# Performance work log

Hardware: AMD Instinct MI355X
Metric: run time of the kernel (lower is better)

The kernel has to match this reference:

```python
import jax, jax.numpy as jnp
import numpy as np

B, S, D = 2, 2048, 1024
H = 16
HD = D // H


def setup_inputs() -> dict:
    key = jax.random.key(0)
    k1, k2, k3 = jax.random.split(key, 3)
    x = jax.random.normal(k1, (B, S, D), dtype=jnp.float32)
    # nn.Linear(d, 3d, bias=False): weight [3d, d]; y = x @ W.T
    w_qkv = jax.random.normal(k2, (3 * D, D), dtype=jnp.float32) * (D ** -0.5)
    w_out = jax.random.normal(k3, (D, D), dtype=jnp.float32) * (D ** -0.5)
    return {"x": x, "w_qkv": w_qkv, "w_out": w_out}


def reference(x, w_qkv, w_out):
    batch, seq_len, _ = x.shape
    qkv = jnp.einsum('bsd,ed->bse', x, w_qkv)  # [B,S,3D]
    q, k, v = jnp.split(qkv, 3, axis=-1)
    # [B,S,D] -> [B,H,S,HD]
    def heads(t):
        return t.reshape(batch, seq_len, H, HD).transpose(0, 2, 1, 3)
    q, k, v = heads(q), heads(k), heads(v)
    scale = HD ** -0.5
    attn = jnp.einsum('bhqd,bhkd->bhqk', q, k) * scale  # [B,H,S,S]
    causal = jnp.triu(jnp.ones((seq_len, seq_len), dtype=bool), k=1)
    attn = jnp.where(causal, -jnp.inf, attn)
    attn = jax.nn.softmax(attn, axis=-1)
    out = jnp.einsum('bhqk,bhkd->bhqd', attn, v)  # [B,H,S,HD]
    out = out.transpose(0, 2, 1, 3).reshape(batch, seq_len, D)
    return jnp.einsum('bsd,ed->bse', out, w_out)
```

## Files before the change

### kernel.cpp

```cpp
#include <hip/hip_runtime.h>

#define NUM_B 2
#define SEQ   2048
#define DIM   1024
#define NH    16
#define HD    64

typedef __attribute__((ext_vector_type(8))) short short8;
typedef __attribute__((ext_vector_type(4))) float floatx4;
typedef unsigned short us;

#define SOFTMAX_SHIFT 12.0f

__device__ __forceinline__ us f2bf(float f) {
    unsigned u = __float_as_uint(f);
    u += 0x7fffu + ((u >> 16) & 1u);
    return (us)(u >> 16);
}
__device__ __forceinline__ us f2bf_t(float f) {
    return (us)(__float_as_uint(f) >> 16);
}

#define GLD16(gptr, lptr) __builtin_amdgcn_global_load_lds( \
    (__attribute__((address_space(1))) unsigned int*)(gptr), \
    (__attribute__((address_space(3))) unsigned int*)(lptr), 16, 0, 0)

__global__ __launch_bounds__(256) void cast_all(
    const float* __restrict__ x, const float* __restrict__ wq,
    const float* __restrict__ wo, us* __restrict__ xb,
    us* __restrict__ wqb, us* __restrict__ wob)
{
    int i = blockIdx.x * 256 + threadIdx.x;
    const float* src; us* dst; int off;
    if (i < 524288)      { src = x;  dst = xb;  off = i; }
    else if (i < 917504) { src = wq; dst = wqb; off = i - 524288; }
    else                 { src = wo; dst = wob; off = i - 917504; }
    const float4* p = (const float4*)src + (size_t)off * 2;
    float4 f0 = p[0];
    float4 f1 = p[1];
    short8 v;
    v[0] = (short)f2bf(f0.x); v[1] = (short)f2bf(f0.y);
    v[2] = (short)f2bf(f0.z); v[3] = (short)f2bf(f0.w);
    v[4] = (short)f2bf(f1.x); v[5] = (short)f2bf(f1.y);
    v[6] = (short)f2bf(f1.z); v[7] = (short)f2bf(f1.w);
    *(short8*)(dst + (size_t)off * 8) = v;
}

__global__ __launch_bounds__(256, 2) void gemm_qkv(
    const us* __restrict__ A, const us* __restrict__ Bw,
    us* __restrict__ qb, us* __restrict__ kb, us* __restrict__ vt)
{
    __shared__ us As[128 * 64];
    __shared__ us Bs[128 * 64];
    const int t = threadIdx.x;
    const int lane = t & 63, w = t >> 6;
    const int l16 = lane & 15, quad = lane >> 4;
    const int wr = (w >> 1) * 64, wc = (w & 1) * 64;
    const int m0 = blockIdx.y * 128, n0 = blockIdx.x * 128;
    const bool isV = (blockIdx.x >= 16);
    const int srow = lane >> 3;
    const int soff = ((lane & 7) ^ srow) << 3;
    const int rsw  = l16 & 7;

    floatx4 acc[4][4];
    #pragma unroll
    for (int i = 0; i < 4; ++i)
        #pragma unroll
        for (int j = 0; j < 4; ++j) acc[i][j] = (floatx4){0.f, 0.f, 0.f, 0.f};

    for (int k0 = 0; k0 < DIM; k0 += 64) {
        #pragma unroll
        for (int c = 0; c < 4; ++c) {
            int chunk = w * 4 + c;
            int row = chunk * 8 + srow;
            GLD16(A  + (size_t)(m0 + row) * DIM + k0 + soff, &As[chunk * 512]);
            GLD16(Bw + (size_t)(n0 + row) * DIM + k0 + soff, &Bs[chunk * 512]);
        }
        __syncthreads();
        #pragma unroll
        for (int s = 0; s < 2; ++s) {
            short8 af[4], bf[4];
            #pragma unroll
            for (int i = 0; i < 4; ++i)
                af[i] = *(const short8*)&As[(wr + i * 16 + l16) * 64 + (((s * 4 + quad) ^ rsw) << 3)];
            #pragma unroll
            for (int j = 0; j < 4; ++j)
                bf[j] = *(const short8*)&Bs[(wc + j * 16 + l16) * 64 + (((s * 4 + quad) ^ rsw) << 3)];
            if (!isV) {
                #pragma unroll
                for (int i = 0; i < 4; ++i)
                    #pragma unroll
                    for (int j = 0; j < 4; ++j)
                        acc[i][j] = __builtin_amdgcn_mfma_f32_16x16x32_bf16(af[i], bf[j], acc[i][j], 0, 0, 0);
            } else {
                #pragma unroll
                for (int i = 0; i < 4; ++i)
                    #pragma unroll
                    for (int j = 0; j < 4; ++j)
                        acc[i][j] = __builtin_amdgcn_mfma_f32_16x16x32_bf16(bf[j], af[i], acc[i][j], 0, 0, 0);
            }
        }
        __syncthreads();
    }

    if (!isV) {
        const int which = n0 >> 10;
        const float sc = (which == 0) ? 0.125f : 1.0f;
        us* dst = (which == 0) ? qb : kb;
        #pragma unroll
        for (int i = 0; i < 4; ++i) {
            #pragma unroll
            for (int j = 0; j < 4; ++j) {
                int e = n0 + wc + j * 16 + l16;
                int h  = (e >> 6) & 15;
                int hd = e & 63;
                #pragma unroll
                for (int r = 0; r < 4; ++r) {
                    int m = m0 + wr + i * 16 + quad * 4 + r;
                    int b = m >> 11, s = m & 2047;
                    dst[((size_t)((b * NH + h) * SEQ + s) << 6) + hd] = f2bf(acc[i][j][r] * sc);
                }
            }
        }
    } else {
        #pragma unroll
        for (int i = 0; i < 4; ++i) {
            int m = m0 + wr + i * 16 + l16;
            int b = m >> 11, s = m & 2047;
            #pragma unroll
            for (int j = 0; j < 4; ++j) {
                int e0 = (n0 - 2048) + wc + j * 16 + quad * 4;
                #pragma unroll
                for (int r = 0; r < 4; ++r) {
                    int e = e0 + r;
                    int h = e >> 6, hd = e & 63;
                    vt[((size_t)((b * NH + h) * HD + hd) << 11) + s] = f2bf(acc[i][j][r]);
                }
            }
        }
    }
}

__global__ __launch_bounds__(256, 2) void gemm_out(
    const us* __restrict__ A, const us* __restrict__ Bw, float* __restrict__ outp)
{
    __shared__ us As[64 * 64];
    __shared__ us Bs[128 * 64];
    const int t = threadIdx.x;
    const int lane = t & 63, w = t >> 6;
    const int l16 = lane & 15, quad = lane >> 4;
    const int wr = (w >> 1) * 32, wc = (w & 1) * 64;
    const int m0 = blockIdx.y * 64, n0 = blockIdx.x * 128;
    const int srow = lane >> 3;
    const int soff = ((lane & 7) ^ srow) << 3;
    const int rsw  = l16 & 7;

    floatx4 acc[2][4];
    #pragma unroll
    for (int i = 0; i < 2; ++i)
        #pragma unroll
        for (int j = 0; j < 4; ++j) acc[i][j] = (floatx4){0.f, 0.f, 0.f, 0.f};

    for (int k0 = 0; k0 < DIM; k0 += 64) {
        #pragma unroll
        for (int c = 0; c < 2; ++c) {
            int chunk = w * 2 + c;
            int row = chunk * 8 + srow;
            GLD16(A + (size_t)(m0 + row) * DIM + k0 + soff, &As[chunk * 512]);
        }
        #pragma unroll
        for (int c = 0; c < 4; ++c) {
            int chunk = w * 4 + c;
            int row = chunk * 8 + srow;
            GLD16(Bw + (size_t)(n0 + row) * DIM + k0 + soff, &Bs[chunk * 512]);
        }
        __syncthreads();
        #pragma unroll
        for (int s = 0; s < 2; ++s) {
            short8 af[2], bf[4];
            #pragma unroll
            for (int i = 0; i < 2; ++i)
                af[i] = *(const short8*)&As[(wr + i * 16 + l16) * 64 + (((s * 4 + quad) ^ rsw) << 3)];
            #pragma unroll
            for (int j = 0; j < 4; ++j)
                bf[j] = *(const short8*)&Bs[(wc + j * 16 + l16) * 64 + (((s * 4 + quad) ^ rsw) << 3)];
            #pragma unroll
            for (int i = 0; i < 2; ++i)
                #pragma unroll
                for (int j = 0; j < 4; ++j)
                    acc[i][j] = __builtin_amdgcn_mfma_f32_16x16x32_bf16(af[i], bf[j], acc[i][j], 0, 0, 0);
        }
        __syncthreads();
    }

    #pragma unroll
    for (int i = 0; i < 2; ++i)
        #pragma unroll
        for (int j = 0; j < 4; ++j) {
            int n = n0 + wc + j * 16 + l16;
            #pragma unroll
            for (int r = 0; r < 4; ++r) {
                int m = m0 + wr + i * 16 + quad * 4 + r;
                outp[(size_t)m * DIM + n] = acc[i][j][r];
            }
        }
}

__global__ __launch_bounds__(256, 4) void attn(
    const us* __restrict__ qb, const us* __restrict__ kb,
    const us* __restrict__ vt, us* __restrict__ ob)
{
    __shared__ us Ks[2][64 * 64];
    __shared__ us Vs[2][64 * 64];
    __shared__ us Ps[4 * 16 * 72];
    const int t = threadIdx.x;
    const int lane = t & 63, w = t >> 6;
    const int l16 = lane & 15, quad = lane >> 4;
    const int idx = blockIdx.x;
    const int qt = 31 - (idx >> 5);
    const int bh = idx & 31;
    const int b = bh >> 4, h = bh & 15;
    const int q0 = qt << 6;
    const int r0 = q0 + w * 16;
    const int rowb = r0 + quad * 4;
    const size_t base = (size_t)bh * SEQ * HD;
    const us* qbh = qb + base;
    const us* kbh = kb + base;
    const us* vth = vt + base;
    us* Pp = Ps + w * 16 * 72;
    const int srow = lane >> 3;
    const int soff = ((lane & 7) ^ srow) << 3;
    const int rsw  = l16 & 7;

    short8 qa[2];
    #pragma unroll
    for (int s = 0; s < 2; ++s)
        qa[s] = *(const short8*)(qbh + (size_t)(r0 + l16) * HD + s * 32 + quad * 8);

    floatx4 o[4];
    #pragma unroll
    for (int j = 0; j < 4; ++j) o[j] = (floatx4){0.f, 0.f, 0.f, 0.f};
    float lrow[4] = {0.f, 0.f, 0.f, 0.f};

    #pragma unroll
    for (int c = 0; c < 2; ++c) {
        int chunk = w * 2 + c;
        int row = chunk * 8 + srow;
        GLD16(kbh + (size_t)row * HD + soff, &Ks[0][chunk * 512]);
        GLD16(vth + (size_t)row * SEQ + soff, &Vs[0][chunk * 512]);
    }
    __syncthreads();

    for (int kt = 0; kt <= qt; ++kt) {
        const int cur = kt & 1;
        if (kt < qt) {
            const int j0n = (kt + 1) << 6;
            #pragma unroll
            for (int c = 0; c < 2; ++c) {
                int chunk = w * 2 + c;
                int row = chunk * 8 + srow;
                GLD16(kbh + (size_t)(j0n + row) * HD + soff, &Ks[cur ^ 1][chunk * 512]);
                GLD16(vth + (size_t)row * SEQ + j0n + soff, &Vs[cur ^ 1][chunk * 512]);
            }
        }

        floatx4 sf[4];
        #pragma unroll
        for (int j = 0; j < 4; ++j)
            sf[j] = (floatx4){-SOFTMAX_SHIFT, -SOFTMAX_SHIFT, -SOFTMAX_SHIFT, -SOFTMAX_SHIFT};
        #pragma unroll
        for (int s = 0; s < 2; ++s)
            #pragma unroll
            for (int j = 0; j < 4; ++j) {
                short8 kf = *(const short8*)&Ks[cur][(j * 16 + l16) * 64 + (((s * 4 + quad) ^ rsw) << 3)];
                sf[j] = __builtin_amdgcn_mfma_f32_16x16x32_bf16(qa[s], kf, sf[j], 0, 0, 0);
            }

        float p[4][4];
        #pragma unroll
        for (int j = 0; j < 4; ++j)
            #pragma unroll
            for (int r = 0; r < 4; ++r) p[j][r] = sf[j][r];

        if (kt == qt) {
            const int j0 = kt << 6;
            #pragma unroll
            for (int j = 0; j < 4; ++j) {
                int colg = j0 + j * 16 + l16;
                #pragma unroll
                for (int r = 0; r < 4; ++r)
                    if (colg > rowb + r) p[j][r] = -1e30f;
            }
        }

        #pragma unroll
        for (int j = 0; j < 4; ++j)
            #pragma unroll
            for (int r = 0; r < 4; ++r) {
                p[j][r] = __expf(p[j][r]);
                Pp[(quad * 4 + r) * 72 + j * 16 + l16] = f2bf_t(p[j][r]);
            }
        #pragma unroll
        for (int r = 0; r < 4; ++r)
            lrow[r] += (p[0][r] + p[1][r]) + (p[2][r] + p[3][r]);

        #pragma unroll
        for (int s = 0; s < 2; ++s) {
            short8 pf = *(const short8*)&Pp[l16 * 72 + s * 32 + quad * 8];
            #pragma unroll
            for (int j = 0; j < 4; ++j) {
                short8 vf = *(const short8*)&Vs[cur][(j * 16 + l16) * 64 + (((s * 4 + quad) ^ rsw) << 3)];
                o[j] = __builtin_amdgcn_mfma_f32_16x16x32_bf16(pf, vf, o[j], 0, 0, 0);
            }
        }
        __syncthreads();
    }

    #pragma unroll
    for (int r = 0; r < 4; ++r) {
        float l = lrow[r];
        l += __shfl_xor(l, 1);
        l += __shfl_xor(l, 2);
        l += __shfl_xor(l, 4);
        l += __shfl_xor(l, 8);
        float inv = 1.0f / l;
        #pragma unroll
        for (int j = 0; j < 4; ++j) {
            float val = o[j][r] * inv;
            ob[(size_t)(b * SEQ + rowb + r) * DIM + h * HD + j * 16 + l16] = f2bf(val);
        }
    }
}

extern "C" void kernel_launch(void* const* d_in, const int* in_sizes, int n_in,
                              void* d_out, int out_size, void* d_ws, size_t ws_size,
                              hipStream_t stream) {
    const float* x     = (const float*)d_in[0];
    const float* w_qkv = (const float*)d_in[1];
    const float* w_out = (const float*)d_in[2];
    float* out = (float*)d_out;
    us* ws = (us*)d_ws;

    const size_t M1 = (size_t)1024 * 1024;
    us* xb  = ws;
    us* wqb = xb  + 4 * M1;
    us* wob = wqb + 3 * M1;
    us* qb  = wob + 1 * M1;
    us* kb  = qb  + 4 * M1;
    us* vt  = kb  + 4 * M1;
    us* obf = vt  + 4 * M1;

    cast_all<<<4096, 256, 0, stream>>>(x, w_qkv, w_out, xb, wqb, wob);
    gemm_qkv<<<dim3(24, 32), 256, 0, stream>>>(xb, wqb, qb, kb, vt);
    attn<<<1024, 256, 0, stream>>>(qb, kb, vt, obf);
    gemm_out<<<dim3(8, 64), 256, 0, stream>>>(obf, wob, out);
}
```

Before: 170.3 us.

## Use 2-wave attention blocks with 32 rows per wave, single-buffered K/V, exp2

The attention kernel now launches 128 threads per block, and each wave handles 32 query rows in two 16-row groups. Each K/V fragment read from LDS is reused for two MFMAs, which halves LDS reads per FLOP. The K/V double buffering is removed: each tile is loaded synchronously before compute, which could expose global-load latency. Q is prescaled by log2(e)/8 in the QKV GEMM so the softmax can use the native exp2 instruction with a matching fixed shift.

```diff
diff --git a/kernel.cpp b/kernel.cpp
--- a/kernel.cpp
+++ b/kernel.cpp
@@ -10,7 +10,14 @@
 typedef __attribute__((ext_vector_type(4))) float floatx4;
 typedef unsigned short us;
 
-#define SOFTMAX_SHIFT 12.0f
+#define QSCALE  0.18033688011112042f
+#define SHIFT2  17.312340490667560f
+
+#if __has_builtin(__builtin_amdgcn_exp2f)
+#define EXP2(x) __builtin_amdgcn_exp2f(x)
+#else
+#define EXP2(x) exp2f(x)
+#endif
 
 __device__ __forceinline__ us f2bf(float f) {
     unsigned u = __float_as_uint(f);
@@ -105,7 +112,7 @@
 
     if (!isV) {
         const int which = n0 >> 10;
-        const float sc = (which == 0) ? 0.125f : 1.0f;
+        const float sc = (which == 0) ? QSCALE : 1.0f;
         us* dst = (which == 0) ? qb : kb;
         #pragma unroll
         for (int i = 0; i < 4; ++i) {
@@ -206,13 +213,13 @@
         }
 }
 
-__global__ __launch_bounds__(256, 4) void attn(
+__global__ __launch_bounds__(128, 3) void attn(
     const us* __restrict__ qb, const us* __restrict__ kb,
     const us* __restrict__ vt, us* __restrict__ ob)
 {
-    __shared__ us Ks[2][64 * 64];
-    __shared__ us Vs[2][64 * 64];
-    __shared__ us Ps[4 * 16 * 72];
+    __shared__ us Ks[64 * 64];
+    __shared__ us Vs[64 * 64];
+    __shared__ us Ps[2 * 32 * 72];
     const int t = threadIdx.x;
     const int lane = t & 63, w = t >> 6;
     const int l16 = lane & 15, quad = lane >> 4;
@@ -221,115 +228,121 @@
     const int bh = idx & 31;
     const int b = bh >> 4, h = bh & 15;
     const int q0 = qt << 6;
-    const int r0 = q0 + w * 16;
-    const int rowb = r0 + quad * 4;
+    const int wrow = q0 + w * 32;
     const size_t base = (size_t)bh * SEQ * HD;
     const us* qbh = qb + base;
     const us* kbh = kb + base;
     const us* vth = vt + base;
-    us* Pp = Ps + w * 16 * 72;
+    us* Pp = Ps + w * 32 * 72;
     const int srow = lane >> 3;
     const int soff = ((lane & 7) ^ srow) << 3;
     const int rsw  = l16 & 7;
 
-    short8 qa[2];
-    #pragma unroll
-    for (int s = 0; s < 2; ++s)
-        qa[s] = *(const short8*)(qbh + (size_t)(r0 + l16) * HD + s * 32 + quad * 8);
-
-    floatx4 o[4];
-    #pragma unroll
-    for (int j = 0; j < 4; ++j) o[j] = (floatx4){0.f, 0.f, 0.f, 0.f};
-    float lrow[4] = {0.f, 0.f, 0.f, 0.f};
-
-    #pragma unroll
-    for (int c = 0; c < 2; ++c) {
-        int chunk = w * 2 + c;
-        int row = chunk * 8 + srow;
-        GLD16(kbh + (size_t)row * HD + soff, &Ks[0][chunk * 512]);
-        GLD16(vth + (size_t)row * SEQ + soff, &Vs[0][chunk * 512]);
+    short8 qa[2][2];
+    #pragma unroll
+    for (int g = 0; g < 2; ++g)
+        #pragma unroll
+        for (int s = 0; s < 2; ++s)
+            qa[g][s] = *(const short8*)(qbh + (size_t)(wrow + g * 16 + l16) * HD + s * 32 + quad * 8);
+
+    floatx4 o[2][4];
+    #pragma unroll
+    for (int g = 0; g < 2; ++g)
+        #pragma unroll
+        for (int j = 0; j < 4; ++j) o[g][j] = (floatx4){0.f, 0.f, 0.f, 0.f};
+    float lrow[2][4] = {};
+
+    for (int kt = 0; kt <= qt; ++kt) {
+        const int j0 = kt << 6;
+        #pragma unroll
+        for (int c = 0; c < 4; ++c) {
+            int chunk = w * 4 + c;
+            int row = chunk * 8 + srow;
+            GLD16(kbh + (size_t)(j0 + row) * HD + soff, &Ks[chunk * 512]);
+            GLD16(vth + (size_t)row * SEQ + j0 + soff, &Vs[chunk * 512]);
+        }
+        __syncthreads();
+
+        floatx4 sf[2][4];
+        #pragma unroll
+        for (int g = 0; g < 2; ++g)
+            #pragma unroll
+            for (int j = 0; j < 4; ++j)
+                sf[g][j] = (floatx4){-SHIFT2, -SHIFT2, -SHIFT2, -SHIFT2};
+        #pragma unroll
+        for (int s = 0; s < 2; ++s)
+            #pragma unroll
+            for (int j = 0; j < 4; ++j) {
+                short8 kf = *(const short8*)&Ks[(j * 16 + l16) * 64 + (((s * 4 + quad) ^ rsw) << 3)];
+                #pragma unroll
+                for (int g = 0; g < 2; ++g)
+                    sf[g][j] = __builtin_amdgcn_mfma_f32_16x16x32_bf16(qa[g][s], kf, sf[g][j], 0, 0, 0);
+            }
+
+        if (kt == qt) {
+            #pragma unroll
+            for (int g = 0; g < 2; ++g) {
+                int rowb = wrow + g * 16 + quad * 4;
+                #pragma unroll
+                for (int j = 0; j < 4; ++j) {
+                    int colg = j0 + j * 16 + l16;
+                    #pragma unroll
+                    for (int r = 0; r < 4; ++r)
+                        if (colg > rowb + r) sf[g][j][r] = -1e30f;
+                }
+            }
+        }
+
+        #pragma unroll
+        for (int g = 0; g < 2; ++g) {
+            float p[4][4];
+            #pragma unroll
+            for (int j = 0; j < 4; ++j)
+                #pragma unroll
+                for (int r = 0; r < 4; ++r) {
+                    p[j][r] = EXP2(sf[g][j][r]);
+                    Pp[(g * 16 + quad * 4 + r) * 72 + j * 16 + l16] = f2bf_t(p[j][r]);
+                }
+            #pragma unroll
+            for (int r = 0; r < 4; ++r)
+                lrow[g][r] += (p[0][r] + p[1][r]) + (p[2][r] + p[3][r]);
+        }
+
+        short8 pf[2][2];
+        #pragma unroll
+        for (int g = 0; g < 2; ++g)
+            #pragma unroll
+            for (int s = 0; s < 2; ++s)
+                pf[g][s] = *(const short8*)&Pp[(g * 16 + l16) * 72 + s * 32 + quad * 8];
+        #pragma unroll
+        for (int s = 0; s < 2; ++s)
+            #pragma unroll
+            for (int j = 0; j < 4; ++j) {
+                short8 vf = *(const short8*)&Vs[(j * 16 + l16) * 64 + (((s * 4 + quad) ^ rsw) << 3)];
+                #pragma unroll
+                for (int g = 0; g < 2; ++g)
+                    o[g][j] = __builtin_amdgcn_mfma_f32_16x16x32_bf16(pf[g][s], vf, o[g][j], 0, 0, 0);
+            }
+        __syncthreads();
     }
-    __syncthreads();
-
-    for (int kt = 0; kt <= qt; ++kt) {
-        const int cur = kt & 1;
-        if (kt < qt) {
-            const int j0n = (kt + 1) << 6;
-            #pragma unroll
-            for (int c = 0; c < 2; ++c) {
-                int chunk = w * 2 + c;
-                int row = chunk * 8 + srow;
-                GLD16(kbh + (size_t)(j0n + row) * HD + soff, &Ks[cur ^ 1][chunk * 512]);
-                GLD16(vth + (size_t)row * SEQ + j0n + soff, &Vs[cur ^ 1][chunk * 512]);
-            }
-        }
-
-        floatx4 sf[4];
-        #pragma unroll
-        for (int j = 0; j < 4; ++j)
-            sf[j] = (floatx4){-SOFTMAX_SHIFT, -SOFTMAX_SHIFT, -SOFTMAX_SHIFT, -SOFTMAX_SHIFT};
-        #pragma unroll
-        for (int s = 0; s < 2; ++s)
-            #pragma unroll
-            for (int j = 0; j < 4; ++j) {
-                short8 kf = *(const short8*)&Ks[cur][(j * 16 + l16) * 64 + (((s * 4 + quad) ^ rsw) << 3)];
-                sf[j] = __builtin_amdgcn_mfma_f32_16x16x32_bf16(qa[s], kf, sf[j], 0, 0, 0);
-            }
-
-        float p[4][4];
-        #pragma unroll
-        for (int j = 0; j < 4; ++j)
-            #pragma unroll
-            for (int r = 0; r < 4; ++r) p[j][r] = sf[j][r];
-
-        if (kt == qt) {
-            const int j0 = kt << 6;
-            #pragma unroll
-            for (int j = 0; j < 4; ++j) {
-                int colg = j0 + j * 16 + l16;
-                #pragma unroll
-                for (int r = 0; r < 4; ++r)
-                    if (colg > rowb + r) p[j][r] = -1e30f;
-            }
-        }
-
-        #pragma unroll
-        for (int j = 0; j < 4; ++j)
-            #pragma unroll
-            for (int r = 0; r < 4; ++r) {
-                p[j][r] = __expf(p[j][r]);
-                Pp[(quad * 4 + r) * 72 + j * 16 + l16] = f2bf_t(p[j][r]);
-            }
-        #pragma unroll
-        for (int r = 0; r < 4; ++r)
-            lrow[r] += (p[0][r] + p[1][r]) + (p[2][r] + p[3][r]);
-
-        #pragma unroll
-        for (int s = 0; s < 2; ++s) {
-            short8 pf = *(const short8*)&Pp[l16 * 72 + s * 32 + quad * 8];
-            #pragma unroll
-            for (int j = 0; j < 4; ++j) {
-                short8 vf = *(const short8*)&Vs[cur][(j * 16 + l16) * 64 + (((s * 4 + quad) ^ rsw) << 3)];
-                o[j] = __builtin_amdgcn_mfma_f32_16x16x32_bf16(pf, vf, o[j], 0, 0, 0);
-            }
-        }
-        __syncthreads();
-    }
-
-    #pragma unroll
-    for (int r = 0; r < 4; ++r) {
-        float l = lrow[r];
-        l += __shfl_xor(l, 1);
-        l += __shfl_xor(l, 2);
-        l += __shfl_xor(l, 4);
-        l += __shfl_xor(l, 8);
-        float inv = 1.0f / l;
-        #pragma unroll
-        for (int j = 0; j < 4; ++j) {
-            float val = o[j][r] * inv;
-            ob[(size_t)(b * SEQ + rowb + r) * DIM + h * HD + j * 16 + l16] = f2bf(val);
-        }
-    }
+
+    #pragma unroll
+    for (int g = 0; g < 2; ++g)
+        #pragma unroll
+        for (int r = 0; r < 4; ++r) {
+            float l = lrow[g][r];
+            l += __shfl_xor(l, 1);
+            l += __shfl_xor(l, 2);
+            l += __shfl_xor(l, 4);
+            l += __shfl_xor(l, 8);
+            float inv = 1.0f / l;
+            int grow = wrow + g * 16 + quad * 4 + r;
+            #pragma unroll
+            for (int j = 0; j < 4; ++j) {
+                float val = o[g][j][r] * inv;
+                ob[(size_t)(b * SEQ + grow) * DIM + h * HD + j * 16 + l16] = f2bf(val);
+            }
+        }
 }
 
 extern "C" void kernel_launch(void* const* d_in, const int* in_sizes, int n_in,
@@ -352,6 +365,6 @@
 
     cast_all<<<4096, 256, 0, stream>>>(x, w_qkv, w_out, xb, wqb, wob);
     gemm_qkv<<<dim3(24, 32), 256, 0, stream>>>(xb, wqb, qb, kb, vt);
-    attn<<<1024, 256, 0, stream>>>(qb, kb, vt, obf);
+    attn<<<1024, 128, 0, stream>>>(qb, kb, vt, obf);
     gemm_out<<<dim3(8, 64), 256, 0, stream>>>(obf, wob, out);
 }
```

After: 176.3 us. +3.5%, slower.
